# Kernel tuning notes

Measured on AMD Instinct MI355X. Metric: run time of the kernel, lower is better.

## Reference

```python
import jax, jax.numpy as jnp
import numpy as np

B, T1, CHUNK = 4, 512, 64
LEFT, RIGHT = 256, 64
T2 = T1 + LEFT + RIGHT          # 832
NPOS = 2 * T1 - 1 + LEFT + RIGHT  # 1343
NFEAT, H, DK = 1024, 16, 64


def setup_inputs() -> dict:
    key = jax.random.key(0)
    ks = jax.random.split(key, 14)
    s = 0.02
    inp = {
        "query":   jax.random.normal(ks[0], (B, T1, NFEAT), jnp.float32),
        "key":     jax.random.normal(ks[1], (B, T2, NFEAT), jnp.float32),
        "value":   jax.random.normal(ks[2], (B, T2, NFEAT), jnp.float32),
        "pos_emb": jax.random.normal(ks[3], (1, NPOS, NFEAT), jnp.float32),
        "Wq":   jax.random.normal(ks[4], (NFEAT, NFEAT), jnp.float32) * s,
        "bq":   jax.random.normal(ks[5], (NFEAT,), jnp.float32) * s,
        "Wk":   jax.random.normal(ks[6], (NFEAT, NFEAT), jnp.float32) * s,
        "bk":   jax.random.normal(ks[7], (NFEAT,), jnp.float32) * s,
        "Wv":   jax.random.normal(ks[8], (NFEAT, NFEAT), jnp.float32) * s,
        "bv":   jax.random.normal(ks[9], (NFEAT,), jnp.float32) * s,
        "Wpos": jax.random.normal(ks[10], (NFEAT, NFEAT), jnp.float32) * s,
        "Wout": jax.random.normal(ks[11], (NFEAT, NFEAT), jnp.float32) * s,
        "bout": jax.random.normal(ks[12], (NFEAT,), jnp.float32) * s,
        "pos_bias_u": jax.random.normal(ks[13], (H, DK), jnp.float32) * s,
        "pos_bias_v": jax.random.normal(jax.random.fold_in(key, 99), (H, DK), jnp.float32) * s,
    }
    # chunk mask with right context: key index j maps to absolute position a = j - LEFT;
    # query i (chunk c = i // CHUNK) may attend a in [c*CHUNK - LEFT, (c+1)*CHUNK + RIGHT)
    c = np.arange(T1) // CHUNK
    a = np.arange(T2) - LEFT
    allowed = (a[None, :] < (c[:, None] + 1) * CHUNK + RIGHT) & (a[None, :] >= c[:, None] * CHUNK - LEFT)
    inp["mask"] = jnp.broadcast_to(jnp.asarray(allowed, dtype=bool)[None], (B, T1, T2))
    inp["left_context_size"] = LEFT
    inp["right_context_size"] = RIGHT
    return inp


def _rel_shift(x, left, right):
    # x: (b, h, t1, 2*t1-1+left+right) -> (b, h, t1, t1+left+right)
    # matches torch as_strided: out[..., i, j] = x[..., i, j - i + t1 - 1]
    b, h, t1, n = x.shape
    t2 = t1 + left + right
    idx = jnp.arange(t2)[None, :] - jnp.arange(t1)[:, None] + (t1 - 1)  # (t1, t2)
    return jnp.take_along_axis(x, idx[None, None], axis=-1)


def reference(query, key, value, pos_emb, mask, Wq, bq, Wk, bk, Wv, bv,
              Wpos, Wout, bout, pos_bias_u, pos_bias_v,
              left_context_size, right_context_size):
    b, t1, _ = query.shape
    q = (query @ Wq.T + bq).reshape(b, t1, H, DK)                       # (b, t1, h, d)
    k = (key @ Wk.T + bk).reshape(b, -1, H, DK).transpose(0, 2, 1, 3)    # (b, h, t2, d)
    v = (value @ Wv.T + bv).reshape(b, -1, H, DK).transpose(0, 2, 1, 3)  # (b, h, t2, d)
    p = (pos_emb @ Wpos.T).reshape(pos_emb.shape[0], -1, H, DK).transpose(0, 2, 1, 3)  # (1, h, n, d)

    q_u = (q + pos_bias_u).transpose(0, 2, 1, 3)   # (b, h, t1, d)
    q_v = (q + pos_bias_v).transpose(0, 2, 1, 3)   # (b, h, t1, d)

    matrix_ac = jnp.einsum('bhqd,bhkd->bhqk', q_u, k)          # (b, h, t1, t2)
    matrix_bd = jnp.einsum('bhqd,ohnd->bhqn', q_v, p)          # (b, h, t1, n)
    matrix_bd = _rel_shift(matrix_bd, left_context_size, right_context_size)

    scores = (matrix_ac + matrix_bd) / jnp.sqrt(jnp.float32(DK))
    m = mask[:, None, :, :]                                    # (b, 1, t1, t2), True = attend
    scores = jnp.where(m, scores, -jnp.inf)
    attn = jax.nn.softmax(scores.astype(jnp.float32), axis=-1).astype(value.dtype)
    attn = jnp.where(m, attn, 0.0)

    x = jnp.einsum('bhqk,bhkd->bqhd', attn, v).reshape(b, t1, H * DK)
    out = x @ Wout.T + bout                                     # (b, t1, n_feat)
    new_cache = jnp.concatenate([k, v], axis=-1)                # (b, h, t2, 2*d)
    return out, new_cache
```

## Files before the change

kernel.cpp:

```cpp
#include <hip/hip_runtime.h>
#include <cstdint>

typedef unsigned short u16;
using short8 = __attribute__((ext_vector_type(8))) short;
using f32x4  = __attribute__((ext_vector_type(4))) float;

#define T1 512
#define T2 832
#define NH 16
#define NPLOC 448

__device__ __forceinline__ u16 f2b(float f){
  union { float f; uint32_t u; } c; c.f = f;
  uint32_t u = c.u;
  u += 0x7fffu + ((u >> 16) & 1u);
  return (u16)(u >> 16);
}
__device__ __forceinline__ float b2f(u16 b){
  union { uint32_t u; float f; } c; c.u = (uint32_t)b << 16; return c.f;
}
__device__ __forceinline__ void async16(const void* g, void* l){
  __builtin_amdgcn_global_load_lds(
      (const __attribute__((address_space(1))) unsigned int*)g,
      (__attribute__((address_space(3))) unsigned int*)l, 16, 0, 0);
}

struct CvtSeg { const float* src; u16* dst; int nblk; };
struct CvtArgs { CvtSeg s[9]; };

__global__ __launch_bounds__(256) void cvt_all(CvtArgs a){
  int rel = blockIdx.x, seg = 0;
  while (rel >= a.s[seg].nblk){ rel -= a.s[seg].nblk; ++seg; }
  int i = rel * 256 + threadIdx.x;
  float4 v = ((const float4*)a.s[seg].src)[i];
  uint64_t p = (uint64_t)f2b(v.x) | ((uint64_t)f2b(v.y) << 16)
             | ((uint64_t)f2b(v.z) << 32) | ((uint64_t)f2b(v.w) << 48);
  *(uint64_t*)(a.s[seg].dst + (size_t)i * 4) = p;
}

__device__ __forceinline__ void gemm_core128(const u16* __restrict__ A, const u16* __restrict__ W,
    int m0, int n0, int tid, f32x4 acc[4][4])
{
  __shared__ __align__(16) u16 As0[4096];
  __shared__ __align__(16) u16 As1[4096];
  __shared__ __align__(16) u16 Bs0[4096];
  __shared__ __align__(16) u16 Bs1[4096];

  int lane = tid & 63, w = tid >> 6;
  int wr = w >> 1, wc = w & 1;
  const int lr = lane & 15, g = lane >> 4;
  const int sslot = (g ^ ((lr >> 1) & 3)) * 8;

  int r = tid >> 2;
  int ssl = ((tid & 3) ^ ((tid >> 3) & 3)) * 8;
  const u16* Asrc = A + (size_t)(m0 + r) * 1024 + ssl;
  const u16* Bsrc = W + (size_t)(n0 + r) * 1024 + ssl;

  auto stage = [&](int k0, u16* as, u16* bs){
    async16(Asrc + k0,         as + tid*8);
    async16(Asrc + 65536 + k0, as + 2048 + tid*8);
    async16(Bsrc + k0,         bs + tid*8);
    async16(Bsrc + 65536 + k0, bs + 2048 + tid*8);
  };

  auto step = [&](u16* as, u16* bs, int kstage, bool do_stage, bool last){
    if (last) asm volatile("s_waitcnt vmcnt(0)" ::: "memory");
    else      asm volatile("s_waitcnt vmcnt(4)" ::: "memory");
    __builtin_amdgcn_sched_barrier(0);
    __builtin_amdgcn_s_barrier();
    __builtin_amdgcn_sched_barrier(0);
    short8 a[4], b[4];
    #pragma unroll
    for (int m = 0; m < 4; ++m) a[m] = *(const short8*)&as[(wr*64 + m*16 + lr)*32 + sslot];
    #pragma unroll
    for (int n = 0; n < 4; ++n) b[n] = *(const short8*)&bs[(wc*64 + n*16 + lr)*32 + sslot];
    asm volatile("s_waitcnt lgkmcnt(0)" ::: "memory");
    __builtin_amdgcn_sched_barrier(0);
    __builtin_amdgcn_s_barrier();
    __builtin_amdgcn_sched_barrier(0);
    if (do_stage) stage(kstage, as, bs);
    __builtin_amdgcn_sched_barrier(0);
    __builtin_amdgcn_s_setprio(1);
    #pragma unroll
    for (int m = 0; m < 4; ++m)
      #pragma unroll
      for (int n = 0; n < 4; ++n)
        acc[m][n] = __builtin_amdgcn_mfma_f32_16x16x32_bf16(a[m], b[n], acc[m][n], 0, 0, 0);
    __builtin_amdgcn_s_setprio(0);
  };

  stage(0,  As0, Bs0);
  stage(32, As1, Bs1);
  for (int it = 0; it < 16; ++it){
    step(As0, Bs0, it*64 + 64, it < 15, false);
    step(As1, Bs1, it*64 + 96, it < 15, it == 15);
  }
}

struct G4Args {
  const u16 *q, *k, *v, *p;
  const u16 *Wq, *Wk, *Wv, *Wp;
  const float *bq, *bk, *bv, *pbu, *pbv;
  u16 *qu, *qv2, *katt, *vatt, *patt;
  float *cache;
};

__global__ __launch_bounds__(256, 4) void gemm4(G4Args ga){
  int bid0 = blockIdx.x;
  int bid = (bid0 & 7) * 72 + (bid0 >> 3);
  int tid = threadIdx.x;
  int mode, mb; const u16 *A, *W;
  if (bid < 128)      { mode = 0; mb = bid >> 3;         A = ga.q; W = ga.Wq; }
  else if (bid < 336) { mode = 1; mb = (bid - 128) >> 3; A = ga.k; W = ga.Wk; }
  else if (bid < 544) { mode = 2; mb = (bid - 336) >> 3; A = ga.v; W = ga.Wv; }
  else                { mode = 3; mb = (bid - 544) >> 3; A = ga.p; W = ga.Wp; }
  int m0 = mb * 128, n0 = (bid & 7) * 128;
  f32x4 acc[4][4] = {};
  gemm_core128(A, W, m0, n0, tid, acc);

  int lane = tid & 63, w = tid >> 6;
  int wr = w >> 1, wc = w & 1;
  const int lr = lane & 15, g = lane >> 4;
  #pragma unroll
  for (int m = 0; m < 4; ++m){
    #pragma unroll
    for (int n = 0; n < 4; ++n){
      #pragma unroll
      for (int j = 0; j < 4; ++j){
        int row = m0 + wr*64 + m*16 + g*4 + j;
        int col = n0 + wc*64 + n*16 + lr;
        float vv = acc[m][n][j];
        if (mode == 0){
          vv += ga.bq[col];
          int h = col >> 6, d = col & 63, b_ = row >> 9, t = row & 511;
          size_t o = ((size_t)((b_*NH + h)*T1 + t))*64 + d;
          ga.qu [o] = f2b(vv + ga.pbu[col]);
          ga.qv2[o] = f2b(vv + ga.pbv[col]);
        } else if (mode == 1 || mode == 2){
          vv += (mode == 1 ? ga.bk : ga.bv)[col];
          int h = col >> 6, d = col & 63;
          int b_ = row / T2, t2 = row - b_*T2;
          size_t base = (size_t)(b_*NH + h)*T2 + t2;
          ga.cache[base*128 + (mode == 2 ? 64 : 0) + d] = vv;
          (mode == 1 ? ga.katt : ga.vatt)[base*64 + d] = f2b(vv);
        } else {
          if (row < NPLOC){
            int h = col >> 6, d = col & 63;
            ga.patt[((size_t)h*NPLOC + row)*64 + d] = f2b(vv);
          }
        }
      }
    }
  }
}

__global__ __launch_bounds__(256, 4) void gemm_out(const u16* __restrict__ A, const u16* __restrict__ W,
                                                   const float* __restrict__ bias, float* __restrict__ out){
  int bid0 = blockIdx.x;
  int bid = (bid0 & 7) * 16 + (bid0 >> 3);
  int m0 = (bid >> 3) * 128, n0 = (bid & 7) * 128;
  int tid = threadIdx.x;
  f32x4 acc[4][4] = {};
  gemm_core128(A, W, m0, n0, tid, acc);
  int lane = tid & 63, w = tid >> 6;
  int wr = w >> 1, wc = w & 1;
  const int lr = lane & 15, g = lane >> 4;
  #pragma unroll
  for (int m = 0; m < 4; ++m)
    #pragma unroll
    for (int n = 0; n < 4; ++n)
      #pragma unroll
      for (int j = 0; j < 4; ++j){
        int row = m0 + wr*64 + m*16 + g*4 + j;
        int col = n0 + wc*64 + n*16 + lr;
        out[(size_t)row*1024 + col] = acc[m][n][j] + bias[col];
      }
}

__global__ __launch_bounds__(256, 2) void attn_v2(
    const u16* __restrict__ qu, const u16* __restrict__ qv,
    const u16* __restrict__ katt, const u16* __restrict__ vatt,
    const u16* __restrict__ patt, u16* __restrict__ xout)
{
  __shared__ __align__(16) u16 SB[64*384];
  __shared__ __align__(16) u16 STG[14336];
  int tid = threadIdx.x, lane = tid & 63, w = tid >> 6;
  int bid0 = blockIdx.x;
  int bid = (bid0 & 7) * 64 + (bid0 >> 3);
  int c = bid & 7, h = (bid >> 3) & 15, b = bid >> 7;
  int bh = b*NH + h;
  const int lr = lane & 15, g = lane >> 4, lk = g * 8;

  auto sb_off = [&](int r, int cc) -> uint32_t {
    return ((uint32_t)(r*384 + cc)*2) ^ ((uint32_t)(r & 15) << 4);
  };
  auto stg_swz = [&](uint32_t o) -> uint32_t { return o ^ (((o >> 7) & 7u) << 4); };
  auto vt_off = [&](int d, int kk) -> uint32_t {
    return ((uint32_t)(d*192 + kk)*2) ^ ((uint32_t)(((d & 7) ^ ((d >> 3) & 7))) << 4);
  };

  int qrow = 16*w + lr;
  const u16* qub = qu + ((size_t)bh*T1 + c*64 + qrow)*64;
  const u16* qvb = qv + ((size_t)bh*T1 + c*64 + qrow)*64;
  short8 qu0 = *(const short8*)(qub + lk);
  short8 qu1 = *(const short8*)(qub + 32 + lk);
  short8 qv0 = *(const short8*)(qvb + lk);
  short8 qv1 = *(const short8*)(qvb + 32 + lk);

  const char* psrc = (const char*)(patt + (size_t)h*NPLOC*64);
  for (int pc = 0; pc < 2; ++pc){
    #pragma unroll
    for (int i = 0; i < 7; ++i){
      uint32_t o = (uint32_t)(i*256 + tid)*16;
      async16(psrc + pc*28672 + stg_swz(o), (char*)STG + o);
    }
    __syncthreads();
    for (int nt = 0; nt < 14; ++nt){
      uint32_t bo = (uint32_t)((nt*16 + lr)*64)*2;
      short8 b0 = *(const short8*)((const char*)STG + stg_swz(bo + lk*2));
      short8 b1 = *(const short8*)((const char*)STG + stg_swz(bo + (32 + lk)*2));
      f32x4 acc = {0.f,0.f,0.f,0.f};
      __builtin_amdgcn_s_setprio(1);
      acc = __builtin_amdgcn_mfma_f32_16x16x32_bf16(qv0, b0, acc, 0, 0, 0);
      acc = __builtin_amdgcn_mfma_f32_16x16x32_bf16(qv1, b1, acc, 0, 0, 0);
      __builtin_amdgcn_s_setprio(0);
      int nl = pc*224 + nt*16 + lr;
      #pragma unroll
      for (int j = 0; j < 4; ++j){
        int r = 16*w + g*4 + j;
        int jj = nl + r - 63;
        if (jj >= 0 && jj < 384) *(u16*)((char*)SB + sb_off(r, jj)) = f2b(acc[j]);
      }
    }
    __syncthreads();
  }

  const char* ksrc = (const char*)(katt + ((size_t)bh*T2 + c*64)*64);
  f32x4 accs[24];
  #pragma unroll
  for (int t = 0; t < 24; ++t) accs[t] = (f32x4){0.f,0.f,0.f,0.f};
  #pragma unroll
  for (int kc = 0; kc < 2; ++kc){
    #pragma unroll
    for (int i = 0; i < 6; ++i){
      uint32_t o = (uint32_t)(i*256 + tid)*16;
      async16(ksrc + kc*24576 + stg_swz(o), (char*)STG + o);
    }
    __syncthreads();
    #pragma unroll
    for (int nt = 0; nt < 12; ++nt){
      uint32_t bo = (uint32_t)((nt*16 + lr)*64)*2;
      short8 b0 = *(const short8*)((const char*)STG + stg_swz(bo + lk*2));
      short8 b1 = *(const short8*)((const char*)STG + stg_swz(bo + (32 + lk)*2));
      int t = kc*12 + nt;
      __builtin_amdgcn_s_setprio(1);
      accs[t] = __builtin_amdgcn_mfma_f32_16x16x32_bf16(qu0, b0, accs[t], 0, 0, 0);
      accs[t] = __builtin_amdgcn_mfma_f32_16x16x32_bf16(qu1, b1, accs[t], 0, 0, 0);
      __builtin_amdgcn_s_setprio(0);
    }
    __syncthreads();
  }

  #pragma unroll
  for (int t = 0; t < 24; ++t)
    #pragma unroll
    for (int j = 0; j < 4; ++j){
      int r = 16*w + g*4 + j, cc = t*16 + lr;
      accs[t][j] += b2f(*(const u16*)((const char*)SB + sb_off(r, cc)));
    }
  float mx[4] = {-1e30f,-1e30f,-1e30f,-1e30f};
  #pragma unroll
  for (int t = 0; t < 24; ++t)
    #pragma unroll
    for (int j = 0; j < 4; ++j) mx[j] = fmaxf(mx[j], accs[t][j]);
  #pragma unroll
  for (int j = 0; j < 4; ++j){
    mx[j] = fmaxf(mx[j], __shfl_xor(mx[j], 1));
    mx[j] = fmaxf(mx[j], __shfl_xor(mx[j], 2));
    mx[j] = fmaxf(mx[j], __shfl_xor(mx[j], 4));
    mx[j] = fmaxf(mx[j], __shfl_xor(mx[j], 8));
  }
  float sm[4] = {0.f,0.f,0.f,0.f};
  #pragma unroll
  for (int t = 0; t < 24; ++t)
    #pragma unroll
    for (int j = 0; j < 4; ++j){
      accs[t][j] = __expf((accs[t][j] - mx[j]) * 0.125f);
      sm[j] += accs[t][j];
    }
  #pragma unroll
  for (int j = 0; j < 4; ++j){
    sm[j] += __shfl_xor(sm[j], 1);
    sm[j] += __shfl_xor(sm[j], 2);
    sm[j] += __shfl_xor(sm[j], 4);
    sm[j] += __shfl_xor(sm[j], 8);
    sm[j] = 1.f / sm[j];
  }
  #pragma unroll
  for (int t = 0; t < 24; ++t)
    #pragma unroll
    for (int j = 0; j < 4; ++j){
      int r = 16*w + g*4 + j, cc = t*16 + lr;
      *(u16*)((char*)SB + sb_off(r, cc)) = f2b(accs[t][j] * sm[j]);
    }
  __syncthreads();

  f32x4 acco[4] = {};
  #pragma unroll
  for (int vc = 0; vc < 2; ++vc){
    if (vc) __syncthreads();
    const u16* vb = vatt + ((size_t)bh*T2 + c*64 + vc*192)*64;
    #pragma unroll
    for (int i = 0; i < 6; ++i){
      int e = (i*256 + tid)*8;
      int kk = e >> 6, d0 = e & 63;
      uint4 vv4 = *(const uint4*)(vb + (size_t)kk*64 + d0);
      u16 uu[8] = { (u16)(vv4.x & 0xffff), (u16)(vv4.x >> 16), (u16)(vv4.y & 0xffff), (u16)(vv4.y >> 16),
                    (u16)(vv4.z & 0xffff), (u16)(vv4.z >> 16), (u16)(vv4.w & 0xffff), (u16)(vv4.w >> 16) };
      #pragma unroll
      for (int j = 0; j < 8; ++j)
        *(u16*)((char*)STG + vt_off(d0 + j, kk)) = uu[j];
    }
    __syncthreads();
    #pragma unroll
    for (int kt = 0; kt < 6; ++kt){
      short8 a = *(const short8*)((const char*)SB + sb_off(16*w + lr, vc*192 + kt*32 + lk));
      __builtin_amdgcn_s_setprio(1);
      #pragma unroll
      for (int n = 0; n < 4; ++n){
        short8 bb = *(const short8*)((const char*)STG + vt_off(n*16 + lr, kt*32 + lk));
        acco[n] = __builtin_amdgcn_mfma_f32_16x16x32_bf16(a, bb, acco[n], 0, 0, 0);
      }
      __builtin_amdgcn_s_setprio(0);
    }
  }

  #pragma unroll
  for (int n = 0; n < 4; ++n)
    #pragma unroll
    for (int j = 0; j < 4; ++j){
      int r = 16*w + g*4 + j;
      int t = c*64 + r, d = n*16 + lr;
      xout[((size_t)b*T1 + t)*1024 + h*64 + d] = f2b(acco[n][j]);
    }
}

extern "C" void kernel_launch(void* const* d_in, const int* in_sizes, int n_in,
                              void* d_out, int out_size, void* d_ws, size_t ws_size,
                              hipStream_t stream)
{
  const float* query = (const float*)d_in[0];
  const float* key   = (const float*)d_in[1];
  const float* value = (const float*)d_in[2];
  const float* pos   = (const float*)d_in[3];
  const float* Wq  = (const float*)d_in[4];
  const float* bq  = (const float*)d_in[5];
  const float* Wk  = (const float*)d_in[6];
  const float* bk  = (const float*)d_in[7];
  const float* Wv  = (const float*)d_in[8];
  const float* bv  = (const float*)d_in[9];
  const float* Wp  = (const float*)d_in[10];
  const float* Wo  = (const float*)d_in[11];
  const float* bo  = (const float*)d_in[12];
  const float* pbu = (const float*)d_in[13];
  const float* pbv = (const float*)d_in[14];

  float* out   = (float*)d_out;
  float* cache = out + 2097152;

  u16* ws     = (u16*)d_ws;
  u16* q_bf   = ws;
  u16* key_bf = ws + 2097152;
  u16* val_bf = ws + 5505024;
  u16* pos_bf = ws + 8912896;
  u16* Wq_bf  = ws + 9437184;
  u16* Wk_bf  = ws + 10485760;
  u16* Wv_bf  = ws + 11534336;
  u16* Wp_bf  = ws + 12582912;
  u16* Wo_bf  = ws + 13631488;
  u16* qu_bf  = ws + 14680064;
  u16* qv_bf  = ws + 16777216;
  u16* katt   = ws + 18874368;
  u16* vatt   = ws + 22282240;
  u16* patt   = ws + 25690112;
  u16* x_bf   = ws + 26148864;

  CvtArgs ca;
  ca.s[0] = { query,            q_bf,   2048 };
  ca.s[1] = { key,              key_bf, 3328 };
  ca.s[2] = { value,            val_bf, 3328 };
  ca.s[3] = { Wq,               Wq_bf,  1024 };
  ca.s[4] = { Wk,               Wk_bf,  1024 };
  ca.s[5] = { Wv,               Wv_bf,  1024 };
  ca.s[6] = { Wp,               Wp_bf,  1024 };
  ca.s[7] = { Wo,               Wo_bf,  1024 };
  ca.s[8] = { pos + 448*1024,   pos_bf, 448 };
  cvt_all<<<14272, 256, 0, stream>>>(ca);

  G4Args ga;
  ga.q = q_bf; ga.k = key_bf; ga.v = val_bf; ga.p = pos_bf;
  ga.Wq = Wq_bf; ga.Wk = Wk_bf; ga.Wv = Wv_bf; ga.Wp = Wp_bf;
  ga.bq = bq; ga.bk = bk; ga.bv = bv; ga.pbu = pbu; ga.pbv = pbv;
  ga.qu = qu_bf; ga.qv2 = qv_bf; ga.katt = katt; ga.vatt = vatt; ga.patt = patt;
  ga.cache = cache;
  gemm4<<<576, 256, 0, stream>>>(ga);

  attn_v2<<<512, 256, 0, stream>>>(qu_bf, qv_bf, katt, vatt, patt, x_bf);

  gemm_out<<<128, 256, 0, stream>>>(x_bf, Wo_bf, bo, out);
}
```

Baseline: 92.53 us.

## Triple-buffer GEMM LDS pipeline and split output GEMM into 64-row tiles

```diff
diff --git a/kernel.cpp b/kernel.cpp
--- a/kernel.cpp
+++ b/kernel.cpp
@@ -43,8 +43,10 @@
 {
   __shared__ __align__(16) u16 As0[4096];
   __shared__ __align__(16) u16 As1[4096];
+  __shared__ __align__(16) u16 As2[4096];
   __shared__ __align__(16) u16 Bs0[4096];
   __shared__ __align__(16) u16 Bs1[4096];
+  __shared__ __align__(16) u16 Bs2[4096];
 
   int lane = tid & 63, w = tid >> 6;
   int wr = w >> 1, wc = w & 1;
@@ -63,7 +65,8 @@
     async16(Bsrc + 65536 + k0, bs + 2048 + tid*8);
   };
 
-  auto step = [&](u16* as, u16* bs, int kstage, bool do_stage, bool last){
+  auto step = [&](const u16* as, const u16* bs, u16* sas, u16* sbs,
+                  int kstage, bool do_stage, bool last){
     if (last) asm volatile("s_waitcnt vmcnt(0)" ::: "memory");
     else      asm volatile("s_waitcnt vmcnt(4)" ::: "memory");
     __builtin_amdgcn_sched_barrier(0);
@@ -74,12 +77,7 @@
     for (int m = 0; m < 4; ++m) a[m] = *(const short8*)&as[(wr*64 + m*16 + lr)*32 + sslot];
     #pragma unroll
     for (int n = 0; n < 4; ++n) b[n] = *(const short8*)&bs[(wc*64 + n*16 + lr)*32 + sslot];
-    asm volatile("s_waitcnt lgkmcnt(0)" ::: "memory");
-    __builtin_amdgcn_sched_barrier(0);
-    __builtin_amdgcn_s_barrier();
-    __builtin_amdgcn_sched_barrier(0);
-    if (do_stage) stage(kstage, as, bs);
-    __builtin_amdgcn_sched_barrier(0);
+    if (do_stage) stage(kstage, sas, sbs);
     __builtin_amdgcn_s_setprio(1);
     #pragma unroll
     for (int m = 0; m < 4; ++m)
@@ -87,14 +85,79 @@
       for (int n = 0; n < 4; ++n)
         acc[m][n] = __builtin_amdgcn_mfma_f32_16x16x32_bf16(a[m], b[n], acc[m][n], 0, 0, 0);
     __builtin_amdgcn_s_setprio(0);
+    asm volatile("s_waitcnt lgkmcnt(0)" ::: "memory");
+    __builtin_amdgcn_sched_barrier(0);
   };
 
   stage(0,  As0, Bs0);
   stage(32, As1, Bs1);
-  for (int it = 0; it < 16; ++it){
-    step(As0, Bs0, it*64 + 64, it < 15, false);
-    step(As1, Bs1, it*64 + 96, it < 15, it == 15);
-  }
+  for (int s = 0; s < 30; s += 3){
+    step(As0, Bs0, As2, Bs2, (s+2)*32, true, false);
+    step(As1, Bs1, As0, Bs0, (s+3)*32, true, false);
+    step(As2, Bs2, As1, Bs1, (s+4)*32, true, false);
+  }
+  step(As0, Bs0, As2, Bs2, 0, false, false);
+  step(As1, Bs1, As2, Bs2, 0, false, true);
+}
+
+__device__ __forceinline__ void gemm_core64(const u16* __restrict__ A, const u16* __restrict__ W,
+    int m0, int n0, int tid, f32x4 acc[4][2])
+{
+  __shared__ __align__(16) u16 As0[2048];
+  __shared__ __align__(16) u16 As1[2048];
+  __shared__ __align__(16) u16 As2[2048];
+  __shared__ __align__(16) u16 Bs0[4096];
+  __shared__ __align__(16) u16 Bs1[4096];
+  __shared__ __align__(16) u16 Bs2[4096];
+
+  int lane = tid & 63, wc = tid >> 6;
+  const int lr = lane & 15, g = lane >> 4;
+  const int sslot = (g ^ ((lr >> 1) & 3)) * 8;
+
+  int r = tid >> 2;
+  int ssl = ((tid & 3) ^ ((tid >> 3) & 3)) * 8;
+  const u16* Asrc = A + (size_t)(m0 + r) * 1024 + ssl;
+  const u16* Bsrc = W + (size_t)(n0 + r) * 1024 + ssl;
+
+  auto stage = [&](int k0, u16* as, u16* bs){
+    async16(Asrc + k0,         as + tid*8);
+    async16(Bsrc + k0,         bs + tid*8);
+    async16(Bsrc + 65536 + k0, bs + 2048 + tid*8);
+  };
+
+  auto step = [&](const u16* as, const u16* bs, u16* sas, u16* sbs,
+                  int kstage, bool do_stage, bool last){
+    if (last) asm volatile("s_waitcnt vmcnt(0)" ::: "memory");
+    else      asm volatile("s_waitcnt vmcnt(3)" ::: "memory");
+    __builtin_amdgcn_sched_barrier(0);
+    __builtin_amdgcn_s_barrier();
+    __builtin_amdgcn_sched_barrier(0);
+    short8 a[4], b[2];
+    #pragma unroll
+    for (int m = 0; m < 4; ++m) a[m] = *(const short8*)&as[(m*16 + lr)*32 + sslot];
+    #pragma unroll
+    for (int n = 0; n < 2; ++n) b[n] = *(const short8*)&bs[(wc*32 + n*16 + lr)*32 + sslot];
+    if (do_stage) stage(kstage, sas, sbs);
+    __builtin_amdgcn_s_setprio(1);
+    #pragma unroll
+    for (int m = 0; m < 4; ++m)
+      #pragma unroll
+      for (int n = 0; n < 2; ++n)
+        acc[m][n] = __builtin_amdgcn_mfma_f32_16x16x32_bf16(a[m], b[n], acc[m][n], 0, 0, 0);
+    __builtin_amdgcn_s_setprio(0);
+    asm volatile("s_waitcnt lgkmcnt(0)" ::: "memory");
+    __builtin_amdgcn_sched_barrier(0);
+  };
+
+  stage(0,  As0, Bs0);
+  stage(32, As1, Bs1);
+  for (int s = 0; s < 30; s += 3){
+    step(As0, Bs0, As2, Bs2, (s+2)*32, true, false);
+    step(As1, Bs1, As0, Bs0, (s+3)*32, true, false);
+    step(As2, Bs2, As1, Bs1, (s+4)*32, true, false);
+  }
+  step(As0, Bs0, As2, Bs2, 0, false, false);
+  step(As1, Bs1, As2, Bs2, 0, false, true);
 }
 
 struct G4Args {
@@ -105,7 +168,7 @@
   float *cache;
 };
 
-__global__ __launch_bounds__(256, 4) void gemm4(G4Args ga){
+__global__ __launch_bounds__(256, 3) void gemm4(G4Args ga){
   int bid0 = blockIdx.x;
   int bid = (bid0 & 7) * 72 + (bid0 >> 3);
   int tid = threadIdx.x;
@@ -157,22 +220,21 @@
 __global__ __launch_bounds__(256, 4) void gemm_out(const u16* __restrict__ A, const u16* __restrict__ W,
                                                    const float* __restrict__ bias, float* __restrict__ out){
   int bid0 = blockIdx.x;
-  int bid = (bid0 & 7) * 16 + (bid0 >> 3);
-  int m0 = (bid >> 3) * 128, n0 = (bid & 7) * 128;
+  int bid = (bid0 & 7) * 32 + (bid0 >> 3);
+  int m0 = (bid >> 3) * 64, n0 = (bid & 7) * 128;
   int tid = threadIdx.x;
-  f32x4 acc[4][4] = {};
-  gemm_core128(A, W, m0, n0, tid, acc);
-  int lane = tid & 63, w = tid >> 6;
-  int wr = w >> 1, wc = w & 1;
+  f32x4 acc[4][2] = {};
+  gemm_core64(A, W, m0, n0, tid, acc);
+  int lane = tid & 63, wc = tid >> 6;
   const int lr = lane & 15, g = lane >> 4;
   #pragma unroll
   for (int m = 0; m < 4; ++m)
     #pragma unroll
-    for (int n = 0; n < 4; ++n)
+    for (int n = 0; n < 2; ++n)
       #pragma unroll
       for (int j = 0; j < 4; ++j){
-        int row = m0 + wr*64 + m*16 + g*4 + j;
-        int col = n0 + wc*64 + n*16 + lr;
+        int row = m0 + m*16 + g*4 + j;
+        int col = n0 + wc*32 + n*16 + lr;
         out[(size_t)row*1024 + col] = acc[m][n][j] + bias[col];
       }
 }
@@ -407,5 +469,5 @@
 
   attn_v2<<<512, 256, 0, stream>>>(qu_bf, qv_bf, katt, vatt, patt, x_bf);
 
-  gemm_out<<<128, 256, 0, stream>>>(x_bf, Wo_bf, bo, out);
-}
+  gemm_out<<<256, 256, 0, stream>>>(x_bf, Wo_bf, bo, out);
+}
```

Result: no change. 92.55 us (+0.0%).
